# Kernel tuning notes

Hardware: AMD Instinct MI355X
Metric: run time of the kernel (lower is better)

## Reference

```python
import jax, jax.numpy as jnp
from jax import lax
import numpy as np

T, B, I, H, O = 512, 32, 512, 512, 512


def _gru_layer(x_seq, h0, w_ih, w_hh, b_ih, b_hh, reverse):
    """Single-direction GRU layer, PyTorch gate semantics (r,z,n order).
    x_seq: (T,B,in), h0: (B,H). Returns ys:(T,B,H) in original time order, hT:(B,H)."""
    gi = jnp.einsum('tbi,gi->tbg', x_seq, w_ih) + b_ih  # (T,B,3H) input gates precomputed

    def step(h, gi_t):
        gh = h @ w_hh.T + b_hh
        ir, iz, i_n = jnp.split(gi_t, 3, axis=-1)
        hr, hz, hn = jnp.split(gh, 3, axis=-1)
        r = jax.nn.sigmoid(ir + hr)
        z = jax.nn.sigmoid(iz + hz)
        n = jnp.tanh(i_n + r * hn)
        h_new = (1.0 - z) * n + z * h
        return h_new, h_new

    hT, ys = lax.scan(step, h0, gi, reverse=reverse)
    return ys, hT


def setup_inputs() -> dict:
    key = jax.random.key(0)
    ks = jax.random.split(key, 20)
    s = 1.0 / np.sqrt(H)
    u = lambda k, shape: jax.random.uniform(k, shape, jnp.float32, -s, s)
    inp = {
        'x': jax.random.normal(ks[0], (T, B, I), jnp.float32),
        'h': jnp.zeros((4, B, H), jnp.float32),
        # layer 0 (input I), forward/backward
        'w_ih_0f': u(ks[1], (3 * H, I)), 'w_hh_0f': u(ks[2], (3 * H, H)),
        'b_ih_0f': u(ks[3], (3 * H,)),   'b_hh_0f': u(ks[4], (3 * H,)),
        'w_ih_0b': u(ks[5], (3 * H, I)), 'w_hh_0b': u(ks[6], (3 * H, H)),
        'b_ih_0b': u(ks[7], (3 * H,)),   'b_hh_0b': u(ks[8], (3 * H,)),
        # layer 1 (input 2H)
        'w_ih_1f': u(ks[9], (3 * H, 2 * H)), 'w_hh_1f': u(ks[10], (3 * H, H)),
        'b_ih_1f': u(ks[11], (3 * H,)),      'b_hh_1f': u(ks[12], (3 * H,)),
        'w_ih_1b': u(ks[13], (3 * H, 2 * H)), 'w_hh_1b': u(ks[14], (3 * H, H)),
        'b_ih_1b': u(ks[15], (3 * H,)),       'b_hh_1b': u(ks[16], (3 * H,)),
        # final linear: (O, 2H)
        'fc_w': u(ks[17], (O, 2 * H)), 'fc_b': u(ks[18], (O,)),
    }
    return inp


def reference(x, h,
              w_ih_0f, w_hh_0f, b_ih_0f, b_hh_0f,
              w_ih_0b, w_hh_0b, b_ih_0b, b_hh_0b,
              w_ih_1f, w_hh_1f, b_ih_1f, b_hh_1f,
              w_ih_1b, w_hh_1b, b_ih_1b, b_hh_1b,
              fc_w, fc_b):
    # layer 0: h indices 0 (fwd), 1 (bwd)
    y0f, h0f = _gru_layer(x, h[0], w_ih_0f, w_hh_0f, b_ih_0f, b_hh_0f, reverse=False)
    y0b, h0b = _gru_layer(x, h[1], w_ih_0b, w_hh_0b, b_ih_0b, b_hh_0b, reverse=True)
    x1 = jnp.concatenate([y0f, y0b], axis=-1)  # (T,B,2H)
    # layer 1: h indices 2 (fwd), 3 (bwd)
    y1f, h1f = _gru_layer(x1, h[2], w_ih_1f, w_hh_1f, b_ih_1f, b_hh_1f, reverse=False)
    y1b, h1b = _gru_layer(x1, h[3], w_ih_1b, w_hh_1b, b_ih_1b, b_hh_1b, reverse=True)
    out = jnp.concatenate([y1f, y1b], axis=-1)  # (T,B,2H)
    out = jnp.einsum('tbh,oh->tbo', out, fc_w) + fc_b
    h_n = jnp.stack([h0f, h0b, h1f, h1b], axis=0)  # (4,B,H)
    return out, h_n
```

## Files before the change

### kernel.cpp

```cpp
#include <hip/hip_runtime.h>


typedef unsigned short u16;
typedef __attribute__((ext_vector_type(8))) short bf16x8;
typedef __attribute__((ext_vector_type(4))) float f32x4;

__device__ __forceinline__ u16 f2bf(float f) {
  unsigned u = __float_as_uint(f);
  u += 0x7fffu + ((u >> 16) & 1u);
  return (u16)(u >> 16);
}
__device__ __forceinline__ float bf2f(u16 v) {
  return __uint_as_float((unsigned)v << 16);
}

template<int AUX>
__device__ __forceinline__ void gl_lds16(const void* g, void* l) {
  __builtin_amdgcn_global_load_lds((const __attribute__((address_space(1))) void*)g,
                                   (__attribute__((address_space(3))) void*)l, 16, 0, AUX);
}

__device__ __forceinline__ void st_bf16_cc(u16* p, u16 v) {
  unsigned vv = v;
  asm volatile("global_store_short %0, %1, off sc0 sc1" :: "v"(p), "v"(vv) : "memory");
}
__device__ __forceinline__ void st_u32_cc(unsigned* p, unsigned v) {
  asm volatile("global_store_dword %0, %1, off sc0 sc1" :: "v"(p), "v"(v) : "memory");
}


__global__ void k_zero(unsigned* p, int n) {
  int i = blockIdx.x * blockDim.x + threadIdx.x;
  if (i < n) p[i] = 0u;
}

__global__ void k_cvt(const float* __restrict__ s, u16* __restrict__ d, int n) {
  int i = (blockIdx.x * blockDim.x + threadIdx.x) * 4;
  if (i < n) {
    float4 v = *(const float4*)(s + i);
    unsigned a = (unsigned)f2bf(v.x) | ((unsigned)f2bf(v.y) << 16);
    unsigned b = (unsigned)f2bf(v.z) | ((unsigned)f2bf(v.w) << 16);
    uint2 o; o.x = a; o.y = b;
    *(uint2*)(d + i) = o;
  }
}

__global__ void k_copyf(const float* __restrict__ s, float* __restrict__ d, int n) {
  int i = blockIdx.x * blockDim.x + threadIdx.x;
  if (i < n) d[i] = s[i];
}


template<bool BF16OUT>
__global__ __launch_bounds__(256) void k_gemm(
    const u16* __restrict__ A, const u16* __restrict__ B,
    const float* __restrict__ bias, void* __restrict__ Cv,
    int N, int K)
{
  __shared__ u16 As[128 * 32];
  __shared__ u16 Bs[128 * 32];
  const int tid = threadIdx.x;
  const int w = tid >> 6, l = tid & 63;
  const int bm = blockIdx.x, bn = blockIdx.y;
  const int lj = l & 15, lk = l >> 4;
  const int wm = (w & 1) * 64, wn = (w >> 1) * 64;
  const int srow = l >> 2, scol = (l & 3) * 8;
  f32x4 acc[4][4] = {};
  const u16* Ab = A + (size_t)bm * 128 * K;
  const u16* Bb = B + (size_t)bn * 128 * K;

  for (int kt = 0; kt < K; kt += 32) {
#pragma unroll
    for (int i = 0; i < 2; ++i) {
      int r0 = i * 64 + w * 16;
      gl_lds16<0>(Ab + (size_t)(r0 + srow) * K + kt + scol, &As[r0 * 32]);
      gl_lds16<0>(Bb + (size_t)(r0 + srow) * K + kt + scol, &Bs[r0 * 32]);
    }
    __syncthreads();
    bf16x8 af[4], bf[4];
#pragma unroll
    for (int i = 0; i < 4; ++i) af[i] = *(const bf16x8*)&As[(wm + i * 16 + lj) * 32 + lk * 8];
#pragma unroll
    for (int j = 0; j < 4; ++j) bf[j] = *(const bf16x8*)&Bs[(wn + j * 16 + lj) * 32 + lk * 8];
#pragma unroll
    for (int i = 0; i < 4; ++i)
#pragma unroll
      for (int j = 0; j < 4; ++j)
        acc[i][j] = __builtin_amdgcn_mfma_f32_16x16x32_bf16(af[i], bf[j], acc[i][j], 0, 0, 0);
    __syncthreads();
  }

#pragma unroll
  for (int i = 0; i < 4; ++i)
#pragma unroll
    for (int j = 0; j < 4; ++j) {
      int col = bn * 128 + wn + j * 16 + lj;
      float bv = bias[col];
#pragma unroll
      for (int r2 = 0; r2 < 4; ++r2) {
        int row = bm * 128 + wm + i * 16 + lk * 4 + r2;
        float v = acc[i][j][r2] + bv;
        if (BF16OUT) ((u16*)Cv)[(size_t)row * N + col] = f2bf(v);
        else         ((float*)Cv)[(size_t)row * N + col] = v;
      }
    }
}


#define LSTR 536

__global__ __launch_bounds__(256, 1) void k_gru(
    const u16*  __restrict__ gi,
    const float* __restrict__ whhf,
    const float* __restrict__ whhb,
    const float* __restrict__ bhhf,
    const float* __restrict__ bhhb,
    const float* __restrict__ h0,
    const u16*  __restrict__ hinit,
    u16* __restrict__ y,
    float* __restrict__ hn,
    unsigned* __restrict__ flags)
{
  __shared__ u16 hl[2][32 * LSTR];
  const int tid = threadIdx.x, wg = blockIdx.x;
  const int w = tid >> 6, l = tid & 63;
  const int dir = w >> 1, p = w & 1;
  const int j0 = wg * 32 + p * 16;
  const int lj = l & 15, lk = l >> 4;
  const float* whh = dir ? whhb : whhf;
  const float* bhh = dir ? bhhb : bhhf;

  bf16x8 bfr[3][16];
#pragma unroll
  for (int g = 0; g < 3; ++g) {
    const float* wr = whh + (size_t)(g * 512 + j0 + lj) * 512;
#pragma unroll
    for (int kc = 0; kc < 16; ++kc) {
      const float* s4 = wr + kc * 32 + lk * 8;
      float4 a = *(const float4*)s4;
      float4 b = *(const float4*)(s4 + 4);
      bf16x8 v;
      v[0] = (short)f2bf(a.x); v[1] = (short)f2bf(a.y); v[2] = (short)f2bf(a.z); v[3] = (short)f2bf(a.w);
      v[4] = (short)f2bf(b.x); v[5] = (short)f2bf(b.y); v[6] = (short)f2bf(b.z); v[7] = (short)f2bf(b.w);
      bfr[g][kc] = v;
    }
  }
  float bb[3];
#pragma unroll
  for (int g = 0; g < 3; ++g) bb[g] = bhh[g * 512 + j0 + lj];

  float hreg[2][4];
#pragma unroll
  for (int mt = 0; mt < 2; ++mt)
#pragma unroll
    for (int i = 0; i < 4; ++i)
      hreg[mt][i] = h0[((size_t)dir * 32 + (mt * 16 + lk * 4 + i)) * 512 + j0 + lj];

  for (int s = 0; s < 512; ++s) {
    const int tq = dir ? (511 - s) : s;

    float gg[2][4][3];
#pragma unroll
    for (int mt = 0; mt < 2; ++mt)
#pragma unroll
      for (int i = 0; i < 4; ++i) {
        int b = mt * 16 + lk * 4 + i;
        const u16* gp = gi + ((size_t)tq * 32 + b) * 3072 + dir * 1536 + j0 + lj;
        gg[mt][i][0] = bf2f(gp[0]);
        gg[mt][i][1] = bf2f(gp[512]);
        gg[mt][i][2] = bf2f(gp[1024]);
      }

    if (s > 0) {
      const unsigned ss = (unsigned)s;
      unsigned cap = 0;
      for (;;) {
        unsigned v = __hip_atomic_load(&flags[l & 15], __ATOMIC_RELAXED,
                                       __HIP_MEMORY_SCOPE_AGENT);
        if (__all((int)(v >= ss))) break;
        if (++cap > (1u << 20)) break;
      }
    }

    {
      const u16* src; int rstride, cbase;
      if (s == 0) { src = hinit + (size_t)dir * 32 * 512; rstride = 512; cbase = 0; }
      else { int tp = dir ? (tq + 1) : (tq - 1); src = y + (size_t)tp * 32 * 1024; rstride = 1024; cbase = dir * 512; }
#pragma unroll
      for (int r = 0; r < 16; ++r) {
        int row = p * 16 + r;
        gl_lds16<17>(src + (size_t)row * rstride + cbase + l * 8, &hl[dir][row * LSTR]);
      }
    }
    __syncthreads();

    f32x4 acc[2][3];
#pragma unroll
    for (int mt = 0; mt < 2; ++mt)
#pragma unroll
      for (int g = 0; g < 3; ++g)
        acc[mt][g] = (f32x4){bb[g], bb[g], bb[g], bb[g]};

#pragma unroll
    for (int kc = 0; kc < 16; ++kc) {
      bf16x8 a0 = *(const bf16x8*)&hl[dir][lj * LSTR + kc * 32 + lk * 8];
      bf16x8 a1 = *(const bf16x8*)&hl[dir][(16 + lj) * LSTR + kc * 32 + lk * 8];
#pragma unroll
      for (int g = 0; g < 3; ++g) {
        acc[0][g] = __builtin_amdgcn_mfma_f32_16x16x32_bf16(a0, bfr[g][kc], acc[0][g], 0, 0, 0);
        acc[1][g] = __builtin_amdgcn_mfma_f32_16x16x32_bf16(a1, bfr[g][kc], acc[1][g], 0, 0, 0);
      }
    }
    __syncthreads();

#pragma unroll
    for (int mt = 0; mt < 2; ++mt)
#pragma unroll
      for (int i = 0; i < 4; ++i) {
        int b = mt * 16 + lk * 4 + i;
        float r = 1.f / (1.f + __expf(-(gg[mt][i][0] + acc[mt][0][i])));
        float z = 1.f / (1.f + __expf(-(gg[mt][i][1] + acc[mt][1][i])));
        float nx = gg[mt][i][2] + r * acc[mt][2][i];
        float n = 1.f - 2.f / (1.f + __expf(2.f * nx));
        float h = (1.f - z) * n + z * hreg[mt][i];
        hreg[mt][i] = h;
        st_bf16_cc(y + ((size_t)tq * 32 + b) * 1024 + dir * 512 + j0 + lj, f2bf(h));
        if (s == 511) hn[((size_t)dir * 32 + b) * 512 + j0 + lj] = h;
      }

    asm volatile("s_waitcnt vmcnt(0)" ::: "memory");
    __syncthreads();
    if (tid == 0) st_u32_cc(&flags[wg], (unsigned)(s + 1));
  }
}


extern "C" void kernel_launch(void* const* d_in, const int* in_sizes, int n_in,
                              void* d_out, int out_size, void* d_ws, size_t ws_size,
                              hipStream_t stream)
{
  const float* x     = (const float*)d_in[0];
  const float* h     = (const float*)d_in[1];
  const float* wih0f = (const float*)d_in[2];
  const float* whh0f = (const float*)d_in[3];
  const float* bih0f = (const float*)d_in[4];
  const float* bhh0f = (const float*)d_in[5];
  const float* wih0b = (const float*)d_in[6];
  const float* whh0b = (const float*)d_in[7];
  const float* bih0b = (const float*)d_in[8];
  const float* bhh0b = (const float*)d_in[9];
  const float* wih1f = (const float*)d_in[10];
  const float* whh1f = (const float*)d_in[11];
  const float* bih1f = (const float*)d_in[12];
  const float* bhh1f = (const float*)d_in[13];
  const float* wih1b = (const float*)d_in[14];
  const float* whh1b = (const float*)d_in[15];
  const float* bih1b = (const float*)d_in[16];
  const float* bhh1b = (const float*)d_in[17];
  const float* fcw   = (const float*)d_in[18];
  const float* fcb   = (const float*)d_in[19];
  (void)in_sizes; (void)n_in; (void)out_size;

  char* ws = (char*)d_ws;
  size_t off = 0;
  auto alloc = [&](size_t bytes) { void* p = ws + off; off += (bytes + 255) & ~(size_t)255; return p; };
  u16*      gi    = (u16*)     alloc(16384ull * 3072 * 2);
  u16*      y0    = (u16*)     alloc(16384ull * 1024 * 2);
  char*     y1r   = (char*)    alloc(16384ull * 1024 * 2);
  u16*      Wfc   = (u16*)     alloc(512ull * 1024 * 2);
  u16*      hinit = (u16*)     alloc(4ull * 32 * 512 * 2);
  float*    bias0 = (float*)   alloc(3072 * 4);
  float*    bias1 = (float*)   alloc(3072 * 4);
  unsigned* flags = (unsigned*)alloc(32 * 4);
  size_t need = off;

  if (ws_size < need) {
    hipMemsetAsync(d_out, 0, (size_t)out_size * sizeof(float), stream);
    return;
  }

  u16* y1   = (u16*)y1r;
  u16* xb   = (u16*)y1r;
  u16* Wih0 = (u16*)(y1r + 16777216);
  u16* Wih1 = (u16*)(y1r + 16777216 + 3145728);

  float* out = (float*)d_out;
  float* hn  = out + 512ull * 32 * 512;

  k_zero<<<1, 64, 0, stream>>>(flags, 32);
  auto cvt = [&](const float* s, u16* d, int n) {
    k_cvt<<<dim3((n / 4 + 255) / 256), 256, 0, stream>>>(s, d, n);
  };
  cvt(x, xb, 16384 * 512);
  cvt(wih0f, Wih0, 1536 * 512);
  cvt(wih0b, Wih0 + 1536 * 512, 1536 * 512);
  cvt(wih1f, Wih1, 1536 * 1024);
  cvt(wih1b, Wih1 + 1536 * 1024, 1536 * 1024);
  cvt(fcw, Wfc, 512 * 1024);
  cvt(h, hinit, 4 * 32 * 512);
  k_copyf<<<6, 256, 0, stream>>>(bih0f, bias0, 1536);
  k_copyf<<<6, 256, 0, stream>>>(bih0b, bias0 + 1536, 1536);
  k_copyf<<<6, 256, 0, stream>>>(bih1f, bias1, 1536);
  k_copyf<<<6, 256, 0, stream>>>(bih1b, bias1 + 1536, 1536);

  k_gemm<true><<<dim3(128, 24), 256, 0, stream>>>(xb, Wih0, bias0, gi, 3072, 512);
  k_gru<<<16, 256, 0, stream>>>(gi, whh0f, whh0b, bhh0f, bhh0b,
                                h, hinit, y0, hn, flags);
  k_gemm<true><<<dim3(128, 24), 256, 0, stream>>>(y0, Wih1, bias1, gi, 3072, 1024);
  k_gru<<<16, 256, 0, stream>>>(gi, whh1f, whh1b, bhh1f, bhh1b,
                                h + 2 * 32 * 512, hinit + 2 * 32 * 512,
                                y1, hn + 2ull * 32 * 512, flags + 16);
  k_gemm<false><<<dim3(128, 4), 256, 0, stream>>>(y1, Wfc, fcb, out, 512, 1024);
}
```

Before: 4.844 ms.

## Use per-wave step flags and transposed MFMA output for vectorized gate I/O

```diff
diff --git a/kernel.cpp b/kernel.cpp
--- a/kernel.cpp
+++ b/kernel.cpp
@@ -10,8 +10,8 @@
   u += 0x7fffu + ((u >> 16) & 1u);
   return (u16)(u >> 16);
 }
-__device__ __forceinline__ float bf2f(u16 v) {
-  return __uint_as_float((unsigned)v << 16);
+__device__ __forceinline__ float bf2f(unsigned v) {
+  return __uint_as_float(v << 16);
 }
 
 template<int AUX>
@@ -20,12 +20,11 @@
                                    (__attribute__((address_space(3))) void*)l, 16, 0, AUX);
 }
 
-__device__ __forceinline__ void st_bf16_cc(u16* p, u16 v) {
-  unsigned vv = v;
-  asm volatile("global_store_short %0, %1, off sc0 sc1" :: "v"(p), "v"(vv) : "memory");
-}
 __device__ __forceinline__ void st_u32_cc(unsigned* p, unsigned v) {
   asm volatile("global_store_dword %0, %1, off sc0 sc1" :: "v"(p), "v"(v) : "memory");
+}
+__device__ __forceinline__ void st_u64_cc(void* p, uint2 v) {
+  asm volatile("global_store_dwordx2 %0, %1, off sc0 sc1" :: "v"(p), "v"(v) : "memory");
 }
 
 
@@ -121,14 +120,16 @@
     float* __restrict__ hn,
     unsigned* __restrict__ flags)
 {
-  __shared__ u16 hl[2][32 * LSTR];
+  __shared__ u16 hl[4][32 * LSTR];
   const int tid = threadIdx.x, wg = blockIdx.x;
   const int w = tid >> 6, l = tid & 63;
   const int dir = w >> 1, p = w & 1;
   const int j0 = wg * 32 + p * 16;
   const int lj = l & 15, lk = l >> 4;
+  const int widx = wg * 4 + w;
   const float* whh = dir ? whhb : whhf;
   const float* bhh = dir ? bhhb : bhhf;
+  u16* myl = &hl[w][0];
 
   bf16x8 bfr[3][16];
 #pragma unroll
@@ -145,37 +146,35 @@
       bfr[g][kc] = v;
     }
   }
-  float bb[3];
-#pragma unroll
-  for (int g = 0; g < 3; ++g) bb[g] = bhh[g * 512 + j0 + lj];
+  f32x4 bbv[3];
+#pragma unroll
+  for (int g = 0; g < 3; ++g)
+    bbv[g] = *(const f32x4*)&bhh[g * 512 + j0 + lk * 4];
 
   float hreg[2][4];
 #pragma unroll
-  for (int mt = 0; mt < 2; ++mt)
-#pragma unroll
-    for (int i = 0; i < 4; ++i)
-      hreg[mt][i] = h0[((size_t)dir * 32 + (mt * 16 + lk * 4 + i)) * 512 + j0 + lj];
+  for (int bt = 0; bt < 2; ++bt) {
+    f32x4 hv = *(const f32x4*)&h0[((size_t)dir * 32 + bt * 16 + lj) * 512 + j0 + lk * 4];
+#pragma unroll
+    for (int r = 0; r < 4; ++r) hreg[bt][r] = hv[r];
+  }
 
   for (int s = 0; s < 512; ++s) {
     const int tq = dir ? (511 - s) : s;
 
-    float gg[2][4][3];
-#pragma unroll
-    for (int mt = 0; mt < 2; ++mt)
-#pragma unroll
-      for (int i = 0; i < 4; ++i) {
-        int b = mt * 16 + lk * 4 + i;
-        const u16* gp = gi + ((size_t)tq * 32 + b) * 3072 + dir * 1536 + j0 + lj;
-        gg[mt][i][0] = bf2f(gp[0]);
-        gg[mt][i][1] = bf2f(gp[512]);
-        gg[mt][i][2] = bf2f(gp[1024]);
-      }
+    uint2 gu[2][3];
+#pragma unroll
+    for (int bt = 0; bt < 2; ++bt)
+#pragma unroll
+      for (int g = 0; g < 3; ++g)
+        gu[bt][g] = *(const uint2*)(gi + ((size_t)tq * 32 + bt * 16 + lj) * 3072
+                                    + dir * 1536 + g * 512 + j0 + lk * 4);
 
     if (s > 0) {
       const unsigned ss = (unsigned)s;
       unsigned cap = 0;
       for (;;) {
-        unsigned v = __hip_atomic_load(&flags[l & 15], __ATOMIC_RELAXED,
+        unsigned v = __hip_atomic_load(&flags[l], __ATOMIC_RELAXED,
                                        __HIP_MEMORY_SCOPE_AGENT);
         if (__all((int)(v >= ss))) break;
         if (++cap > (1u << 20)) break;
@@ -187,50 +186,62 @@
       if (s == 0) { src = hinit + (size_t)dir * 32 * 512; rstride = 512; cbase = 0; }
       else { int tp = dir ? (tq + 1) : (tq - 1); src = y + (size_t)tp * 32 * 1024; rstride = 1024; cbase = dir * 512; }
 #pragma unroll
-      for (int r = 0; r < 16; ++r) {
-        int row = p * 16 + r;
-        gl_lds16<17>(src + (size_t)row * rstride + cbase + l * 8, &hl[dir][row * LSTR]);
-      }
-    }
-    __syncthreads();
+      for (int r = 0; r < 32; ++r)
+        gl_lds16<17>(src + (size_t)r * rstride + cbase + l * 8, &myl[r * LSTR]);
+    }
+    asm volatile("s_waitcnt vmcnt(0)" ::: "memory");
+    __builtin_amdgcn_sched_barrier(0);
 
     f32x4 acc[2][3];
 #pragma unroll
-    for (int mt = 0; mt < 2; ++mt)
+    for (int bt = 0; bt < 2; ++bt)
 #pragma unroll
       for (int g = 0; g < 3; ++g)
-        acc[mt][g] = (f32x4){bb[g], bb[g], bb[g], bb[g]};
+        acc[bt][g] = bbv[g];
 
 #pragma unroll
     for (int kc = 0; kc < 16; ++kc) {
-      bf16x8 a0 = *(const bf16x8*)&hl[dir][lj * LSTR + kc * 32 + lk * 8];
-      bf16x8 a1 = *(const bf16x8*)&hl[dir][(16 + lj) * LSTR + kc * 32 + lk * 8];
+      bf16x8 a0 = *(const bf16x8*)&myl[lj * LSTR + kc * 32 + lk * 8];
+      bf16x8 a1 = *(const bf16x8*)&myl[(16 + lj) * LSTR + kc * 32 + lk * 8];
 #pragma unroll
       for (int g = 0; g < 3; ++g) {
-        acc[0][g] = __builtin_amdgcn_mfma_f32_16x16x32_bf16(a0, bfr[g][kc], acc[0][g], 0, 0, 0);
-        acc[1][g] = __builtin_amdgcn_mfma_f32_16x16x32_bf16(a1, bfr[g][kc], acc[1][g], 0, 0, 0);
-      }
-    }
-    __syncthreads();
-
-#pragma unroll
-    for (int mt = 0; mt < 2; ++mt)
-#pragma unroll
-      for (int i = 0; i < 4; ++i) {
-        int b = mt * 16 + lk * 4 + i;
-        float r = 1.f / (1.f + __expf(-(gg[mt][i][0] + acc[mt][0][i])));
-        float z = 1.f / (1.f + __expf(-(gg[mt][i][1] + acc[mt][1][i])));
-        float nx = gg[mt][i][2] + r * acc[mt][2][i];
-        float n = 1.f - 2.f / (1.f + __expf(2.f * nx));
-        float h = (1.f - z) * n + z * hreg[mt][i];
-        hreg[mt][i] = h;
-        st_bf16_cc(y + ((size_t)tq * 32 + b) * 1024 + dir * 512 + j0 + lj, f2bf(h));
-        if (s == 511) hn[((size_t)dir * 32 + b) * 512 + j0 + lj] = h;
-      }
+        acc[0][g] = __builtin_amdgcn_mfma_f32_16x16x32_bf16(bfr[g][kc], a0, acc[0][g], 0, 0, 0);
+        acc[1][g] = __builtin_amdgcn_mfma_f32_16x16x32_bf16(bfr[g][kc], a1, acc[1][g], 0, 0, 0);
+      }
+    }
+
+#pragma unroll
+    for (int bt = 0; bt < 2; ++bt) {
+      const int b = bt * 16 + lj;
+      unsigned q[4];
+      float hv[4];
+#pragma unroll
+      for (int r = 0; r < 4; ++r) {
+        unsigned w0 = (r & 1) ? (((const unsigned*)&gu[bt][0])[r >> 1] >> 16)
+                              : (((const unsigned*)&gu[bt][0])[r >> 1] & 0xffffu);
+        unsigned w1 = (r & 1) ? (((const unsigned*)&gu[bt][1])[r >> 1] >> 16)
+                              : (((const unsigned*)&gu[bt][1])[r >> 1] & 0xffffu);
+        unsigned w2 = (r & 1) ? (((const unsigned*)&gu[bt][2])[r >> 1] >> 16)
+                              : (((const unsigned*)&gu[bt][2])[r >> 1] & 0xffffu);
+        float rr = 1.f / (1.f + __expf(-(bf2f(w0) + acc[bt][0][r])));
+        float zz = 1.f / (1.f + __expf(-(bf2f(w1) + acc[bt][1][r])));
+        float nx = bf2f(w2) + rr * acc[bt][2][r];
+        float nn = 1.f - 2.f / (1.f + __expf(2.f * nx));
+        float h = (1.f - zz) * nn + zz * hreg[bt][r];
+        hreg[bt][r] = h;
+        hv[r] = h;
+        q[r] = (unsigned)f2bf(h);
+      }
+      uint2 pack; pack.x = q[0] | (q[1] << 16); pack.y = q[2] | (q[3] << 16);
+      st_u64_cc(y + ((size_t)tq * 32 + b) * 1024 + dir * 512 + j0 + lk * 4, pack);
+      if (s == 511) {
+        float4 o; o.x = hv[0]; o.y = hv[1]; o.z = hv[2]; o.w = hv[3];
+        *(float4*)&hn[((size_t)dir * 32 + b) * 512 + j0 + lk * 4] = o;
+      }
+    }
 
     asm volatile("s_waitcnt vmcnt(0)" ::: "memory");
-    __syncthreads();
-    if (tid == 0) st_u32_cc(&flags[wg], (unsigned)(s + 1));
+    if (l == 0) st_u32_cc(&flags[widx], (unsigned)(s + 1));
   }
 }
 
@@ -271,7 +282,7 @@
   u16*      hinit = (u16*)     alloc(4ull * 32 * 512 * 2);
   float*    bias0 = (float*)   alloc(3072 * 4);
   float*    bias1 = (float*)   alloc(3072 * 4);
-  unsigned* flags = (unsigned*)alloc(32 * 4);
+  unsigned* flags = (unsigned*)alloc(128 * 4);
   size_t need = off;
 
   if (ws_size < need) {
@@ -287,7 +298,7 @@
   float* out = (float*)d_out;
   float* hn  = out + 512ull * 32 * 512;
 
-  k_zero<<<1, 64, 0, stream>>>(flags, 32);
+  k_zero<<<1, 128, 0, stream>>>(flags, 128);
   auto cvt = [&](const float* s, u16* d, int n) {
     k_cvt<<<dim3((n / 4 + 255) / 256), 256, 0, stream>>>(s, d, n);
   };
@@ -309,6 +320,6 @@
   k_gemm<true><<<dim3(128, 24), 256, 0, stream>>>(y0, Wih1, bias1, gi, 3072, 1024);
   k_gru<<<16, 256, 0, stream>>>(gi, whh1f, whh1b, bhh1f, bhh1b,
                                 h + 2 * 32 * 512, hinit + 2 * 32 * 512,
-                                y1, hn + 2ull * 32 * 512, flags + 16);
+                                y1, hn + 2ull * 32 * 512, flags + 64);
   k_gemm<false><<<dim3(128, 4), 256, 0, stream>>>(y1, Wfc, fcb, out, 512, 1024);
 }
```

Measured after the change: 6.604 ms. 36.3% more time.
